# Kernel tuning notes

Hardware: AMD Instinct MI355X
Metric: run time of the kernel (lower is better)

## Reference

```python
import jax, jax.numpy as jnp
import numpy as np
from jax import lax

INPUT_SIZE = 16
RESERVOIR_SIZE = 1024
OUTPUT_SIZE = 16
SPECTRAL_RADIUS = 0.9
SPARSITY = 0.1
BATCH = 1024
SEQ_LEN = 4096


def setup_inputs() -> dict:
    key = jax.random.key(0)
    k_x, k_win, k_w, k_mask, k_wo, k_b = jax.random.split(key, 6)
    x = jax.random.normal(k_x, (BATCH, SEQ_LEN, INPUT_SIZE), dtype=jnp.float32)
    Win = jax.random.normal(k_win, (RESERVOIR_SIZE, INPUT_SIZE), dtype=jnp.float32)
    W = jax.random.normal(k_w, (RESERVOIR_SIZE, RESERVOIR_SIZE), dtype=jnp.float32)
    # spectral-radius rescaling (done once at init in the torch module)
    eig = np.linalg.eigvals(np.asarray(W))
    W = W * (SPECTRAL_RADIUS / np.max(np.abs(eig))).astype(np.float32)
    # sparsify with Bernoulli(sparsity) mask
    mask = (jax.random.uniform(k_mask, (RESERVOIR_SIZE, RESERVOIR_SIZE)) < SPARSITY).astype(jnp.float32)
    W = W * mask
    Wout_w = jax.random.normal(k_wo, (OUTPUT_SIZE, RESERVOIR_SIZE), dtype=jnp.float32) / np.sqrt(RESERVOIR_SIZE).astype(np.float32)
    Wout_b = jax.random.normal(k_b, (OUTPUT_SIZE,), dtype=jnp.float32) * 0.01
    return {"x": x, "Win": Win, "W": W, "Wout_w": Wout_w, "Wout_b": Wout_b}


def reference(x, Win, W, Wout_w, Wout_b):
    batch = x.shape[0]
    h0 = jnp.zeros((batch, W.shape[0]), dtype=x.dtype)

    def step(h, x_t):
        h = jnp.tanh(x_t @ Win.T + h @ W.T)
        return h, None

    # scan over time: x_time is [seq_len, batch, input_size]
    x_time = jnp.swapaxes(x, 0, 1)
    h_final, _ = lax.scan(step, h0, x_time)
    y = h_final @ Wout_w.T + Wout_b  # [batch, output_size]
    return y
```

## Files before the change

### kernel.cpp

```cpp
#include <hip/hip_runtime.h>

#define RS 1024
#define SL 4096
#define NB 1024
#define NI 16
#define RGRP 32
#define NGRP 32
#define WPG 8

typedef short s8v __attribute__((ext_vector_type(8)));
typedef float f16v __attribute__((ext_vector_type(16)));
typedef unsigned int u4v __attribute__((ext_vector_type(4)));

#define WAIT_VM(N) do { asm volatile("s_waitcnt vmcnt(" #N ")" ::: "memory"); \
                        __builtin_amdgcn_sched_barrier(0); } while (0)

static __device__ __forceinline__ unsigned short f2bf(float f) {
  unsigned u = __float_as_uint(f);
  u += 0x7fffu + ((u >> 16) & 1u);
  return (unsigned short)(u >> 16);
}
static __device__ __forceinline__ float bf2f(unsigned short b) {
  return __uint_as_float(((unsigned)b) << 16);
}
static __device__ __forceinline__ float fast_tanh(float a) {
  float e = __expf(2.0f * a);
  return 1.0f - 2.0f / (e + 1.0f);
}

static __device__ __forceinline__ u4v ld_llc_b128(const void* p) {
  u4v d;
  asm volatile("global_load_dwordx4 %0, %1, off sc0 sc1"
               : "=v"(d) : "v"(p) : "memory");
  return d;
}
static __device__ __forceinline__ void st_llc_b128(void* p, u4v d) {
  asm volatile("global_store_dwordx4 %0, %1, off sc0 sc1"
               : : "v"(p), "v"(d) : "memory");
}

__global__ __launch_bounds__(256) void prep_kernel(
    const float* __restrict__ W, unsigned short* __restrict__ wbf,
    uint4* __restrict__ hA4, int* __restrict__ flags) {
  int idx = blockIdx.x * 256 + threadIdx.x;
  if (idx < RS * RS) wbf[idx] = f2bf(W[idx]);
  if (idx < (NB * RS) / 8) hA4[idx] = make_uint4(0u, 0u, 0u, 0u);
  if (idx < NGRP * 64) flags[idx] = 0;
}

__global__ __launch_bounds__(256, 1) void esn_kernel(
    const float* __restrict__ x, const float* __restrict__ Win,
    const unsigned short* __restrict__ wbf,
    unsigned short* __restrict__ hA, unsigned short* __restrict__ hB,
    int* __restrict__ flags) {
  extern __shared__ char smem[];
  char* hsm = smem;
  char* ctile = smem + 65536;

  const int bid = blockIdx.x;
  const int g = bid & 31;
  const int j = bid >> 5;
  const int tid = threadIdx.x;
  const int w = tid >> 6;
  const int lane = tid & 63;
  const int l31 = lane & 31;
  const int hi = lane >> 5;

  const int n0 = j * 128 + w * 32;
  const int m0 = g * RGRP;

  s8v bw[64];
  {
    const unsigned short* wp = wbf + (size_t)(n0 + l31) * RS + hi * 8;
#pragma unroll
    for (int kk = 0; kk < 64; kk++) bw[kk] = *(const s8v*)(wp + kk * 16);
  }

  union U8 { s8v v; unsigned short u[8]; };
  U8 whi, wlo;
  {
    const float* p = Win + (n0 + l31) * NI + hi * 8;
#pragma unroll
    for (int i = 0; i < 8; i++) {
      float f = p[i];
      unsigned short h16 = f2bf(f);
      whi.u[i] = h16;
      wlo.u[i] = f2bf(f - bf2f(h16));
    }
  }

  int* flag = flags + g * 64;
  const float* xrow = x + (size_t)(m0 + l31) * SL * NI + hi * 8;
  const size_t stg_base = (((size_t)(tid >> 5) * NB) + m0 + (tid & 31)) << 4;
  const char* abase = hsm + hi * 512 + l31 * 16;
  char* wct = ctile + w * 2048;
  int dead = 0;

  for (int t = 0; t < SL; t++) {
    const char* hsrc = (const char*)((t & 1) ? hB : hA);
    char* hdst = (char*)((t & 1) ? hA : hB);

    float4 xa = *(const float4*)(xrow + (size_t)t * NI);
    float4 xb = *(const float4*)(xrow + (size_t)t * NI + 4);

    if (t > 0) {
      if (tid == 0 && !dead) {
        const int target = t * WPG;
        int spins = 0;
        while (__hip_atomic_load(flag, __ATOMIC_RELAXED, __HIP_MEMORY_SCOPE_AGENT) < target) {
          __builtin_amdgcn_s_sleep(8);
          if (++spins > (1 << 16)) { dead = 1; break; }
        }
      }
      __syncthreads();
    }

    {
      u4v stg[16];
#pragma unroll
      for (int q = 0; q < 16; q++)
        stg[q] = ld_llc_b128(hsrc + stg_base + (size_t)q * 131072);
      WAIT_VM(8);
#pragma unroll
      for (int q = 0; q < 8; q++)
        *(u4v*)(hsm + (tid << 4) + q * 4096) = stg[q];
      WAIT_VM(0);
#pragma unroll
      for (int q = 8; q < 16; q++)
        *(u4v*)(hsm + (tid << 4) + q * 4096) = stg[q];
    }

    U8 xhi, xlo;
    {
      float xf[8] = {xa.x, xa.y, xa.z, xa.w, xb.x, xb.y, xb.z, xb.w};
#pragma unroll
      for (int i = 0; i < 8; i++) {
        unsigned short h16 = f2bf(xf[i]);
        xhi.u[i] = h16;
        xlo.u[i] = f2bf(xf[i] - bf2f(h16));
      }
    }
    __syncthreads();

    f16v acc = {};
    acc = __builtin_amdgcn_mfma_f32_32x32x16_bf16(xhi.v, whi.v, acc, 0, 0, 0);
    acc = __builtin_amdgcn_mfma_f32_32x32x16_bf16(xlo.v, whi.v, acc, 0, 0, 0);
    acc = __builtin_amdgcn_mfma_f32_32x32x16_bf16(xhi.v, wlo.v, acc, 0, 0, 0);

#pragma unroll
    for (int kk = 0; kk < 64; kk++) {
      s8v a = *(const s8v*)(abase + kk * 1024);
      acc = __builtin_amdgcn_mfma_f32_32x32x16_bf16(a, bw[kk], acc, 0, 0, 0);
    }

#pragma unroll
    for (int r = 0; r < 16; r++) {
      const int row = (r & 3) + 8 * (r >> 2) + 4 * hi;
      *(unsigned short*)(wct + row * 64 + l31 * 2) = f2bf(fast_tanh(acc[r]));
    }
    asm volatile("s_waitcnt lgkmcnt(0)" ::: "memory");
    __builtin_amdgcn_sched_barrier(0);
    {
      const int row = lane >> 1, c = lane & 1;
      u4v v0 = *(const u4v*)(wct + row * 64 + c * 16);
      u4v v1 = *(const u4v*)(wct + row * 64 + c * 16 + 32);
      char* g0 = hdst + ((((size_t)(n0 >> 3) + c) * NB + m0 + row) << 4);
      char* g1 = hdst + ((((size_t)(n0 >> 3) + c + 2) * NB + m0 + row) << 4);
      st_llc_b128(g0, v0);
      st_llc_b128(g1, v1);
    }
    WAIT_VM(0);
    __syncthreads();
    if (tid == 0)
      __hip_atomic_fetch_add(flag, 1, __ATOMIC_RELAXED, __HIP_MEMORY_SCOPE_AGENT);
  }
}

__global__ __launch_bounds__(256) void yout_kernel(
    const unsigned short* __restrict__ h, const float* __restrict__ Wout,
    const float* __restrict__ bias, float* __restrict__ y) {
  const int tid = threadIdx.x;
  const int b = (blockIdx.x << 4) + (tid >> 4);
  const int o = tid & 15;
  const float* wr = Wout + (o << 10);
  float s = 0.0f;
  for (int k8 = 0; k8 < RS / 8; k8++) {
    const unsigned short* hc = h + (((size_t)k8 * NB + b) << 3);
#pragma unroll
    for (int i = 0; i < 8; i++) s += bf2f(hc[i]) * wr[k8 * 8 + i];
  }
  y[(b << 4) + o] = s + bias[o];
}

extern "C" void kernel_launch(void* const* d_in, const int* in_sizes, int n_in,
                              void* d_out, int out_size, void* d_ws, size_t ws_size,
                              hipStream_t stream) {
  const float* x = (const float*)d_in[0];
  const float* Win = (const float*)d_in[1];
  const float* W = (const float*)d_in[2];
  const float* Wout = (const float*)d_in[3];
  const float* bias = (const float*)d_in[4];
  float* y = (float*)d_out;

  char* ws = (char*)d_ws;
  unsigned short* hA = (unsigned short*)ws;
  unsigned short* hB = (unsigned short*)(ws + (1 << 21));
  unsigned short* wbf = (unsigned short*)(ws + (2 << 21));
  int* flags = (int*)(ws + 3 * (size_t)(1 << 21));

  (void)hipFuncSetAttribute((const void*)esn_kernel,
                            hipFuncAttributeMaxDynamicSharedMemorySize, 73728);

  prep_kernel<<<4096, 256, 0, stream>>>(W, wbf, (uint4*)hA, flags);
  esn_kernel<<<NGRP * WPG, 256, 73728, stream>>>(x, Win, wbf, hA, hB, flags);
  yout_kernel<<<64, 256, 0, stream>>>(hA, Wout, bias, y);
}
```

Baseline: 19.53 ms.

## Split K across waves and reduce partial sums through LDS instead of staging h

Each wave now loads only its quarter of the K dimension of h directly from global memory into registers, and computes partial products for all four 32-column output tiles. Partial accumulators are then exchanged through shared memory and summed by the owning wave. This removes the per-step copy of the full 32x1024 h tile into LDS and the repeated LDS reads of it. In exchange it adds an LDS reduction with extra stores and loads of floats, and it keeps four accumulators live, which raises register pressure.

```diff
diff --git a/kernel.cpp b/kernel.cpp
--- a/kernel.cpp
+++ b/kernel.cpp
@@ -54,7 +54,7 @@
     unsigned short* __restrict__ hA, unsigned short* __restrict__ hB,
     int* __restrict__ flags) {
   extern __shared__ char smem[];
-  char* hsm = smem;
+  char* psm = smem;
   char* ctile = smem + 65536;
 
   const int bid = blockIdx.x;
@@ -69,11 +69,14 @@
   const int n0 = j * 128 + w * 32;
   const int m0 = g * RGRP;
 
-  s8v bw[64];
-  {
-    const unsigned short* wp = wbf + (size_t)(n0 + l31) * RS + hi * 8;
-#pragma unroll
-    for (int kk = 0; kk < 64; kk++) bw[kk] = *(const s8v*)(wp + kk * 16);
+  s8v bw[4][16];
+#pragma unroll
+  for (int idx = 0; idx < 4; idx++) {
+    const int c = (w + idx) & 3;
+    const unsigned short* wp =
+        wbf + (size_t)(j * 128 + c * 32 + l31) * RS + w * 256 + hi * 8;
+#pragma unroll
+    for (int kk = 0; kk < 16; kk++) bw[idx][kk] = *(const s8v*)(wp + kk * 16);
   }
 
   union U8 { s8v v; unsigned short u[8]; };
@@ -91,8 +94,7 @@
 
   int* flag = flags + g * 64;
   const float* xrow = x + (size_t)(m0 + l31) * SL * NI + hi * 8;
-  const size_t stg_base = (((size_t)(tid >> 5) * NB) + m0 + (tid & 31)) << 4;
-  const char* abase = hsm + hi * 512 + l31 * 16;
+  const size_t ab_off = (((size_t)(32 * w + hi) * NB) + m0 + l31) << 4;
   char* wct = ctile + w * 2048;
   int dead = 0;
 
@@ -115,21 +117,6 @@
       __syncthreads();
     }
 
-    {
-      u4v stg[16];
-#pragma unroll
-      for (int q = 0; q < 16; q++)
-        stg[q] = ld_llc_b128(hsrc + stg_base + (size_t)q * 131072);
-      WAIT_VM(8);
-#pragma unroll
-      for (int q = 0; q < 8; q++)
-        *(u4v*)(hsm + (tid << 4) + q * 4096) = stg[q];
-      WAIT_VM(0);
-#pragma unroll
-      for (int q = 8; q < 16; q++)
-        *(u4v*)(hsm + (tid << 4) + q * 4096) = stg[q];
-    }
-
     U8 xhi, xlo;
     {
       float xf[8] = {xa.x, xa.y, xa.z, xa.w, xb.x, xb.y, xb.z, xb.w};
@@ -140,23 +127,61 @@
         xlo.u[i] = f2bf(xf[i] - bf2f(h16));
       }
     }
+    __builtin_amdgcn_sched_barrier(0);
+
+    u4v al[16];
+#pragma unroll
+    for (int kk = 0; kk < 16; kk++)
+      al[kk] = ld_llc_b128(hsrc + ab_off + (size_t)kk * (2 * NB * 16));
+
+    f16v acc[4];
+    {
+      f16v z = {};
+      z = __builtin_amdgcn_mfma_f32_32x32x16_bf16(xhi.v, whi.v, z, 0, 0, 0);
+      z = __builtin_amdgcn_mfma_f32_32x32x16_bf16(xlo.v, whi.v, z, 0, 0, 0);
+      acc[0] = __builtin_amdgcn_mfma_f32_32x32x16_bf16(xhi.v, wlo.v, z, 0, 0, 0);
+      f16v zz = {};
+      acc[1] = zz; acc[2] = zz; acc[3] = zz;
+    }
+
+#define KBLK(K0)                                                            \
+    _Pragma("unroll")                                                       \
+    for (int kk = K0; kk < K0 + 4; kk++) {                                  \
+      union AU { u4v u; s8v s; } au; au.u = al[kk];                         \
+      _Pragma("unroll")                                                     \
+      for (int idx = 0; idx < 4; idx++)                                     \
+        acc[idx] = __builtin_amdgcn_mfma_f32_32x32x16_bf16(au.s, bw[idx][kk], acc[idx], 0, 0, 0); \
+    }
+    WAIT_VM(12); KBLK(0)
+    WAIT_VM(8);  KBLK(4)
+    WAIT_VM(4);  KBLK(8)
+    WAIT_VM(0);  KBLK(12)
+#undef KBLK
+
+#pragma unroll
+    for (int idx = 1; idx < 4; idx++) {
+      const int c = (w + idx) & 3;
+      char* slot = psm + (((c << 2) | w) << 12) + (size_t)l31 * 4;
+#pragma unroll
+      for (int r = 0; r < 16; r++)
+        *(float*)(slot + (hi * 16 + r) * 128) = acc[idx][r];
+    }
     __syncthreads();
 
-    f16v acc = {};
-    acc = __builtin_amdgcn_mfma_f32_32x32x16_bf16(xhi.v, whi.v, acc, 0, 0, 0);
-    acc = __builtin_amdgcn_mfma_f32_32x32x16_bf16(xlo.v, whi.v, acc, 0, 0, 0);
-    acc = __builtin_amdgcn_mfma_f32_32x32x16_bf16(xhi.v, wlo.v, acc, 0, 0, 0);
-
-#pragma unroll
-    for (int kk = 0; kk < 64; kk++) {
-      s8v a = *(const s8v*)(abase + kk * 1024);
-      acc = __builtin_amdgcn_mfma_f32_32x32x16_bf16(a, bw[kk], acc, 0, 0, 0);
+    f16v own = acc[0];
+#pragma unroll
+    for (int idx = 1; idx < 4; idx++) {
+      const int wp = (w + idx) & 3;
+      const char* slot = psm + (((w << 2) | wp) << 12) + (size_t)l31 * 4;
+#pragma unroll
+      for (int r = 0; r < 16; r++)
+        own[r] += *(const float*)(slot + (hi * 16 + r) * 128);
     }
 
 #pragma unroll
     for (int r = 0; r < 16; r++) {
       const int row = (r & 3) + 8 * (r >> 2) + 4 * hi;
-      *(unsigned short*)(wct + row * 64 + l31 * 2) = f2bf(fast_tanh(acc[r]));
+      *(unsigned short*)(wct + row * 64 + l31 * 2) = f2bf(fast_tanh(own[r]));
     }
     asm volatile("s_waitcnt lgkmcnt(0)" ::: "memory");
     __builtin_amdgcn_sched_barrier(0);
```

Result: faster. 17.76 ms (-9.1%).

## Restructure ESN recurrence into two interleaved batch halves with split-K partial reduction

Applied to the files above, without the earlier changes.

Cuts the grid from 256 to 128 blocks. Each block now handles two 32-row batch tiles, one from each half of the batch, and alternates between them so the epilogue and global stores of one tile overlap the MFMA stream of the other. Each wave now takes a K-quarter for all four column chunks and loads h fragments straight from global into registers instead of staging them through LDS. Partial sums are reduced through LDS. Per-tile counters and centralized atomic increments are replaced by per-block flag stores polled on only the two producer blocks each wave needs, which adds LDS reduction traffic and more complex synchronization.

```diff
diff --git a/kernel.cpp b/kernel.cpp
--- a/kernel.cpp
+++ b/kernel.cpp
@@ -4,16 +4,15 @@
 #define SL 4096
 #define NB 1024
 #define NI 16
-#define RGRP 32
-#define NGRP 32
+#define NGP 16
 #define WPG 8
 
 typedef short s8v __attribute__((ext_vector_type(8)));
 typedef float f16v __attribute__((ext_vector_type(16)));
 typedef unsigned int u4v __attribute__((ext_vector_type(4)));
 
-#define WAIT_VM(N) do { asm volatile("s_waitcnt vmcnt(" #N ")" ::: "memory"); \
-                        __builtin_amdgcn_sched_barrier(0); } while (0)
+#define WAIT_VM0 do { asm volatile("s_waitcnt vmcnt(0)" ::: "memory"); \
+                      __builtin_amdgcn_sched_barrier(0); } while (0)
 
 static __device__ __forceinline__ unsigned short f2bf(float f) {
   unsigned u = __float_as_uint(f);
@@ -37,6 +36,16 @@
 static __device__ __forceinline__ void st_llc_b128(void* p, u4v d) {
   asm volatile("global_store_dwordx4 %0, %1, off sc0 sc1"
                : : "v"(p), "v"(d) : "memory");
+}
+static __device__ __forceinline__ void st_llc_b32(void* p, int d) {
+  asm volatile("global_store_dword %0, %1, off sc0 sc1"
+               : : "v"(p), "v"(d) : "memory");
+}
+static __device__ __forceinline__ int ld_llc_b32(const void* p) {
+  int d;
+  asm volatile("global_load_dword %0, %1, off sc0 sc1\n\ts_waitcnt vmcnt(0)"
+               : "=v"(d) : "v"(p) : "memory");
+  return d;
 }
 
 __global__ __launch_bounds__(256) void prep_kernel(
@@ -45,21 +54,21 @@
   int idx = blockIdx.x * 256 + threadIdx.x;
   if (idx < RS * RS) wbf[idx] = f2bf(W[idx]);
   if (idx < (NB * RS) / 8) hA4[idx] = make_uint4(0u, 0u, 0u, 0u);
-  if (idx < NGRP * 64) flags[idx] = 0;
+  if (idx < 4096) flags[idx] = 0;
 }
 
 __global__ __launch_bounds__(256, 1) void esn_kernel(
     const float* __restrict__ x, const float* __restrict__ Win,
     const unsigned short* __restrict__ wbf,
-    unsigned short* __restrict__ hA, unsigned short* __restrict__ hB,
+    unsigned short* __restrict__ h0, unsigned short* __restrict__ h1,
     int* __restrict__ flags) {
   extern __shared__ char smem[];
-  char* hsm = smem;
+  char* psm = smem;
   char* ctile = smem + 65536;
 
   const int bid = blockIdx.x;
-  const int g = bid & 31;
-  const int j = bid >> 5;
+  const int p = bid & 15;
+  const int j = bid >> 4;
   const int tid = threadIdx.x;
   const int w = tid >> 6;
   const int lane = tid & 63;
@@ -67,113 +76,184 @@
   const int hi = lane >> 5;
 
   const int n0 = j * 128 + w * 32;
-  const int m0 = g * RGRP;
-
-  s8v bw[64];
-  {
-    const unsigned short* wp = wbf + (size_t)(n0 + l31) * RS + hi * 8;
-#pragma unroll
-    for (int kk = 0; kk < 64; kk++) bw[kk] = *(const s8v*)(wp + kk * 16);
+  const int m0A = p * 32;
+  const int m0B = m0A + 512;
+
+  s8v bw[4][16];
+#pragma unroll
+  for (int idx = 0; idx < 4; idx++) {
+    const int c = (w + idx) & 3;
+    const unsigned short* wp =
+        wbf + (size_t)(j * 128 + c * 32 + l31) * RS + w * 256 + hi * 8;
+#pragma unroll
+    for (int kk = 0; kk < 16; kk++) bw[idx][kk] = *(const s8v*)(wp + kk * 16);
   }
 
   union U8 { s8v v; unsigned short u[8]; };
   U8 whi, wlo;
   {
-    const float* p = Win + (n0 + l31) * NI + hi * 8;
+    const float* q = Win + (n0 + l31) * NI + hi * 8;
 #pragma unroll
     for (int i = 0; i < 8; i++) {
-      float f = p[i];
+      float f = q[i];
       unsigned short h16 = f2bf(f);
       whi.u[i] = h16;
       wlo.u[i] = f2bf(f - bf2f(h16));
     }
   }
 
-  int* flag = flags + g * 64;
-  const float* xrow = x + (size_t)(m0 + l31) * SL * NI + hi * 8;
-  const size_t stg_base = (((size_t)(tid >> 5) * NB) + m0 + (tid & 31)) << 4;
-  const char* abase = hsm + hi * 512 + l31 * 16;
+  int* flagsA = flags;
+  int* flagsB = flags + 2048;
+  int* myfA = flagsA + ((p * WPG + j) << 4);
+  int* myfB = flagsB + ((p * WPG + j) << 4);
+  const int* pfA0 = flagsA + ((p * WPG + 2 * w) << 4);
+  const int* pfA1 = flagsA + ((p * WPG + 2 * w + 1) << 4);
+  const int* pfB0 = flagsB + ((p * WPG + 2 * w) << 4);
+  const int* pfB1 = flagsB + ((p * WPG + 2 * w + 1) << 4);
+
+  const float* xrowA = x + (size_t)(m0A + l31) * SL * NI + hi * 8;
+  const float* xrowB = x + (size_t)(m0B + l31) * SL * NI + hi * 8;
+  const size_t abA = (((size_t)(32 * w + hi) * NB) + m0A + l31) << 4;
+  const size_t abB = abA + ((size_t)512 << 4);
   char* wct = ctile + w * 2048;
   int dead = 0;
 
-  for (int t = 0; t < SL; t++) {
-    const char* hsrc = (const char*)((t & 1) ? hB : hA);
-    char* hdst = (char*)((t & 1) ? hA : hB);
-
-    float4 xa = *(const float4*)(xrow + (size_t)t * NI);
-    float4 xb = *(const float4*)(xrow + (size_t)t * NI + 4);
-
-    if (t > 0) {
-      if (tid == 0 && !dead) {
-        const int target = t * WPG;
-        int spins = 0;
-        while (__hip_atomic_load(flag, __ATOMIC_RELAXED, __HIP_MEMORY_SCOPE_AGENT) < target) {
-          __builtin_amdgcn_s_sleep(8);
-          if (++spins > (1 << 16)) { dead = 1; break; }
-        }
-      }
-      __syncthreads();
+#define POLL(F0, F1, TGT)                                                   \
+  if (lane == 0 && !dead) {                                                 \
+    int spins = 0;                                                          \
+    while (ld_llc_b32(F0) < (TGT) || ld_llc_b32(F1) < (TGT)) {              \
+      __builtin_amdgcn_s_sleep(2);                                          \
+      if (++spins > (1 << 14)) { dead = 1; break; }                         \
+    }                                                                       \
+  }
+
+#define ISSUE_AL(AL, SRC, AB)                                               \
+  _Pragma("unroll")                                                         \
+  for (int kk = 0; kk < 16; kk++)                                           \
+    AL[kk] = ld_llc_b128((SRC) + (AB) + (size_t)kk * (2 * NB * 16));
+
+#define XFRAG(XA0, XA1, XH, XL)                                             \
+  {                                                                         \
+    float xf[8] = {XA0.x, XA0.y, XA0.z, XA0.w, XA1.x, XA1.y, XA1.z, XA1.w}; \
+    _Pragma("unroll")                                                       \
+    for (int i = 0; i < 8; i++) {                                           \
+      unsigned short h16 = f2bf(xf[i]);                                     \
+      XH.u[i] = h16;                                                        \
+      XL.u[i] = f2bf(xf[i] - bf2f(h16));                                    \
+    }                                                                       \
+  }
+
+#define MFMA_STREAM(AL, XH, XL, ACC)                                        \
+  {                                                                         \
+    f16v z = {};                                                            \
+    z = __builtin_amdgcn_mfma_f32_32x32x16_bf16(XH.v, whi.v, z, 0, 0, 0);   \
+    z = __builtin_amdgcn_mfma_f32_32x32x16_bf16(XL.v, whi.v, z, 0, 0, 0);   \
+    ACC[0] = __builtin_amdgcn_mfma_f32_32x32x16_bf16(XH.v, wlo.v, z, 0, 0, 0); \
+    f16v zz = {};                                                           \
+    ACC[1] = zz; ACC[2] = zz; ACC[3] = zz;                                  \
+  }                                                                         \
+  _Pragma("unroll")                                                         \
+  for (int kk = 0; kk < 16; kk++) {                                         \
+    union AU { u4v u; s8v s; } au; au.u = AL[kk];                           \
+    _Pragma("unroll")                                                       \
+    for (int idx = 0; idx < 4; idx++)                                       \
+      ACC[idx] = __builtin_amdgcn_mfma_f32_32x32x16_bf16(au.s, bw[idx][kk], ACC[idx], 0, 0, 0); \
+  }
+
+#define PARTIAL_WRITE(ACC)                                                  \
+  _Pragma("unroll")                                                         \
+  for (int idx = 1; idx < 4; idx++) {                                       \
+    const int c = (w + idx) & 3;                                            \
+    char* slot = psm + (((c << 2) | w) << 12) + (size_t)l31 * 4;            \
+    _Pragma("unroll")                                                       \
+    for (int r = 0; r < 16; r++)                                            \
+      *(float*)(slot + (hi * 16 + r) * 128) = ACC[idx][r];                  \
+  }
+
+#define REDUCE_EPI(ACC, M0, HD)                                             \
+  {                                                                         \
+    f16v own = ACC[0];                                                      \
+    _Pragma("unroll")                                                       \
+    for (int idx = 1; idx < 4; idx++) {                                     \
+      const int wp2 = (w + idx) & 3;                                        \
+      const char* slot = psm + (((w << 2) | wp2) << 12) + (size_t)l31 * 4;  \
+      _Pragma("unroll")                                                     \
+      for (int r = 0; r < 16; r++)                                          \
+        own[r] += *(const float*)(slot + (hi * 16 + r) * 128);              \
+    }                                                                       \
+    _Pragma("unroll")                                                       \
+    for (int r = 0; r < 16; r++) {                                          \
+      const int row = (r & 3) + 8 * (r >> 2) + 4 * hi;                      \
+      *(unsigned short*)(wct + row * 64 + l31 * 2) = f2bf(fast_tanh(own[r])); \
+    }                                                                       \
+    asm volatile("s_waitcnt lgkmcnt(0)" ::: "memory");                      \
+    __builtin_amdgcn_sched_barrier(0);                                      \
+    const int row = lane >> 1, c = lane & 1;                                \
+    u4v v0 = *(const u4v*)(wct + row * 64 + c * 16);                        \
+    u4v v1 = *(const u4v*)(wct + row * 64 + c * 16 + 32);                   \
+    char* g0 = (HD) + ((((size_t)(n0 >> 3) + c) * NB + (M0) + row) << 4);   \
+    char* g1 = (HD) + ((((size_t)(n0 >> 3) + c + 2) * NB + (M0) + row) << 4); \
+    st_llc_b128(g0, v0);                                                    \
+    st_llc_b128(g1, v1);                                                    \
+  }
+
+  u4v alA[16], alB[16];
+  float4 xa0, xa1, xb0, xb1;
+  ISSUE_AL(alB, (const char*)h0, abB)
+  ISSUE_AL(alA, (const char*)h0, abA)
+  xa0 = *(const float4*)(xrowA);
+  xa1 = *(const float4*)(xrowA + 4);
+  xb0 = *(const float4*)(xrowB);
+  xb1 = *(const float4*)(xrowB + 4);
+
+  for (int it = 0; it < SL; it++) {
+    const char* hsrc = (const char*)((it & 1) ? h1 : h0);
+    char* hdst = (char*)((it & 1) ? h0 : h1);
+    (void)hsrc;
+
+    WAIT_VM0;
+    U8 xh, xl;
+    XFRAG(xa0, xa1, xh, xl)
+    f16v acc[4];
+    MFMA_STREAM(alA, xh, xl, acc)
+
+    PARTIAL_WRITE(acc)
+    __syncthreads();
+    REDUCE_EPI(acc, m0A, hdst)
+
+    XFRAG(xb0, xb1, xh, xl)
+    MFMA_STREAM(alB, xh, xl, acc)
+    __syncthreads();
+
+    PARTIAL_WRITE(acc)
+    WAIT_VM0;
+    __syncthreads();
+    if (tid == 0) st_llc_b32(myfA, it + 1);
+    REDUCE_EPI(acc, m0B, hdst)
+
+    POLL(pfA0, pfA1, it + 1)
+
+    WAIT_VM0;
+    __syncthreads();
+    if (tid == 0) st_llc_b32(myfB, it + 1);
+
+    POLL(pfB0, pfB1, it + 1)
+    ISSUE_AL(alB, hdst, abB)
+    ISSUE_AL(alA, hdst, abA)
+    {
+      const size_t xo = (size_t)((it + 1 < SL) ? it + 1 : 0) * NI;
+      xa0 = *(const float4*)(xrowA + xo);
+      xa1 = *(const float4*)(xrowA + xo + 4);
+      xb0 = *(const float4*)(xrowB + xo);
+      xb1 = *(const float4*)(xrowB + xo + 4);
     }
-
-    {
-      u4v stg[16];
-#pragma unroll
-      for (int q = 0; q < 16; q++)
-        stg[q] = ld_llc_b128(hsrc + stg_base + (size_t)q * 131072);
-      WAIT_VM(8);
-#pragma unroll
-      for (int q = 0; q < 8; q++)
-        *(u4v*)(hsm + (tid << 4) + q * 4096) = stg[q];
-      WAIT_VM(0);
-#pragma unroll
-      for (int q = 8; q < 16; q++)
-        *(u4v*)(hsm + (tid << 4) + q * 4096) = stg[q];
-    }
-
-    U8 xhi, xlo;
-    {
-      float xf[8] = {xa.x, xa.y, xa.z, xa.w, xb.x, xb.y, xb.z, xb.w};
-#pragma unroll
-      for (int i = 0; i < 8; i++) {
-        unsigned short h16 = f2bf(xf[i]);
-        xhi.u[i] = h16;
-        xlo.u[i] = f2bf(xf[i] - bf2f(h16));
-      }
-    }
-    __syncthreads();
-
-    f16v acc = {};
-    acc = __builtin_amdgcn_mfma_f32_32x32x16_bf16(xhi.v, whi.v, acc, 0, 0, 0);
-    acc = __builtin_amdgcn_mfma_f32_32x32x16_bf16(xlo.v, whi.v, acc, 0, 0, 0);
-    acc = __builtin_amdgcn_mfma_f32_32x32x16_bf16(xhi.v, wlo.v, acc, 0, 0, 0);
-
-#pragma unroll
-    for (int kk = 0; kk < 64; kk++) {
-      s8v a = *(const s8v*)(abase + kk * 1024);
-      acc = __builtin_amdgcn_mfma_f32_32x32x16_bf16(a, bw[kk], acc, 0, 0, 0);
-    }
-
-#pragma unroll
-    for (int r = 0; r < 16; r++) {
-      const int row = (r & 3) + 8 * (r >> 2) + 4 * hi;
-      *(unsigned short*)(wct + row * 64 + l31 * 2) = f2bf(fast_tanh(acc[r]));
-    }
-    asm volatile("s_waitcnt lgkmcnt(0)" ::: "memory");
-    __builtin_amdgcn_sched_barrier(0);
-    {
-      const int row = lane >> 1, c = lane & 1;
-      u4v v0 = *(const u4v*)(wct + row * 64 + c * 16);
-      u4v v1 = *(const u4v*)(wct + row * 64 + c * 16 + 32);
-      char* g0 = hdst + ((((size_t)(n0 >> 3) + c) * NB + m0 + row) << 4);
-      char* g1 = hdst + ((((size_t)(n0 >> 3) + c + 2) * NB + m0 + row) << 4);
-      st_llc_b128(g0, v0);
-      st_llc_b128(g1, v1);
-    }
-    WAIT_VM(0);
-    __syncthreads();
-    if (tid == 0)
-      __hip_atomic_fetch_add(flag, 1, __ATOMIC_RELAXED, __HIP_MEMORY_SCOPE_AGENT);
-  }
+  }
+#undef POLL
+#undef ISSUE_AL
+#undef XFRAG
+#undef MFMA_STREAM
+#undef PARTIAL_WRITE
+#undef REDUCE_EPI
 }
 
 __global__ __launch_bounds__(256) void yout_kernel(
@@ -203,15 +283,15 @@
   float* y = (float*)d_out;
 
   char* ws = (char*)d_ws;
-  unsigned short* hA = (unsigned short*)ws;
-  unsigned short* hB = (unsigned short*)(ws + (1 << 21));
+  unsigned short* h0 = (unsigned short*)ws;
+  unsigned short* h1 = (unsigned short*)(ws + (1 << 21));
   unsigned short* wbf = (unsigned short*)(ws + (2 << 21));
   int* flags = (int*)(ws + 3 * (size_t)(1 << 21));
 
   (void)hipFuncSetAttribute((const void*)esn_kernel,
                             hipFuncAttributeMaxDynamicSharedMemorySize, 73728);
 
-  prep_kernel<<<4096, 256, 0, stream>>>(W, wbf, (uint4*)hA, flags);
-  esn_kernel<<<NGRP * WPG, 256, 73728, stream>>>(x, Win, wbf, hA, hB, flags);
-  yout_kernel<<<64, 256, 0, stream>>>(hA, Wout, bias, y);
-}
+  prep_kernel<<<4096, 256, 0, stream>>>(W, wbf, (uint4*)h0, flags);
+  esn_kernel<<<NGP * WPG, 256, 73728, stream>>>(x, Win, wbf, h0, h1, flags);
+  yout_kernel<<<64, 256, 0, stream>>>(h0, Wout, bias, y);
+}
```

Measured after the change: 55.89 ms. 2.86x slower.

## Split-K recurrence with two interleaved batch halves and per-wave flag polling

Applied to the files above, without the earlier changes.

Restructures the persistent ESN kernel so each block owns 64 output columns for 16 partitions, with waves splitting the K dimension and reducing partials through LDS. The batch is split into two halves processed alternately, so the global-memory load of one half's state overlaps the compute and sync of the other. Hidden-state fragments are loaded directly from global memory into registers, skipping the LDS staging step. The single atomic counter per group is replaced by per-wave flag words polled with vector loads. This aims to hide the step-to-step sync latency, at the cost of the LDS reduction and a more complex flag protocol.

```diff
diff --git a/kernel.cpp b/kernel.cpp
--- a/kernel.cpp
+++ b/kernel.cpp
@@ -4,9 +4,6 @@
 #define SL 4096
 #define NB 1024
 #define NI 16
-#define RGRP 32
-#define NGRP 32
-#define WPG 8
 
 typedef short s8v __attribute__((ext_vector_type(8)));
 typedef float f16v __attribute__((ext_vector_type(16)));
@@ -34,146 +31,241 @@
                : "=v"(d) : "v"(p) : "memory");
   return d;
 }
+static __device__ __forceinline__ u4v ld_llc_b128_sync(const void* p) {
+  u4v d;
+  asm volatile("global_load_dwordx4 %0, %1, off sc0 sc1\n\ts_waitcnt vmcnt(0)"
+               : "=v"(d) : "v"(p) : "memory");
+  return d;
+}
 static __device__ __forceinline__ void st_llc_b128(void* p, u4v d) {
   asm volatile("global_store_dwordx4 %0, %1, off sc0 sc1"
                : : "v"(p), "v"(d) : "memory");
 }
+static __device__ __forceinline__ void st_llc_b32(void* p, int d) {
+  asm volatile("global_store_dword %0, %1, off sc0 sc1"
+               : : "v"(p), "v"(d) : "memory");
+}
+static __device__ __forceinline__ int min16v(u4v a, u4v b, u4v c, u4v d) {
+  int m = min(min(min((int)a.x, (int)a.y), min((int)a.z, (int)a.w)),
+              min(min((int)b.x, (int)b.y), min((int)b.z, (int)b.w)));
+  int n = min(min(min((int)c.x, (int)c.y), min((int)c.z, (int)c.w)),
+              min(min((int)d.x, (int)d.y), min((int)d.z, (int)d.w)));
+  return min(m, n);
+}
+static __device__ __forceinline__ void poll_issue(const void* p, u4v& a, u4v& b,
+                                                  u4v& c, u4v& d) {
+  asm volatile("global_load_dwordx4 %0, %4, off sc0 sc1\n\t"
+               "global_load_dwordx4 %1, %4, off offset:16 sc0 sc1\n\t"
+               "global_load_dwordx4 %2, %4, off offset:32 sc0 sc1\n\t"
+               "global_load_dwordx4 %3, %4, off offset:48 sc0 sc1"
+               : "=v"(a), "=v"(b), "=v"(c), "=v"(d) : "v"(p) : "memory");
+}
+static __device__ __forceinline__ int min16_block(const void* p) {
+  u4v a, b, c, d;
+  asm volatile("global_load_dwordx4 %0, %4, off sc0 sc1\n\t"
+               "global_load_dwordx4 %1, %4, off offset:16 sc0 sc1\n\t"
+               "global_load_dwordx4 %2, %4, off offset:32 sc0 sc1\n\t"
+               "global_load_dwordx4 %3, %4, off offset:48 sc0 sc1\n\t"
+               "s_waitcnt vmcnt(0)"
+               : "=v"(a), "=v"(b), "=v"(c), "=v"(d) : "v"(p) : "memory");
+  return min16v(a, b, c, d);
+}
 
 __global__ __launch_bounds__(256) void prep_kernel(
     const float* __restrict__ W, unsigned short* __restrict__ wbf,
-    uint4* __restrict__ hA4, int* __restrict__ flags) {
+    char* __restrict__ h0, int* __restrict__ flags) {
   int idx = blockIdx.x * 256 + threadIdx.x;
   if (idx < RS * RS) wbf[idx] = f2bf(W[idx]);
-  if (idx < (NB * RS) / 8) hA4[idx] = make_uint4(0u, 0u, 0u, 0u);
-  if (idx < NGRP * 64) flags[idx] = 0;
+  if (idx < (NB * RS) / 8) {
+    u4v z = {0u, 0u, 0u, 0u};
+    st_llc_b128(h0 + (size_t)idx * 16, z);
+  }
+  if (idx < 2048) st_llc_b32(flags + idx, 0);
 }
 
 __global__ __launch_bounds__(256, 1) void esn_kernel(
     const float* __restrict__ x, const float* __restrict__ Win,
     const unsigned short* __restrict__ wbf,
-    unsigned short* __restrict__ hA, unsigned short* __restrict__ hB,
+    unsigned short* __restrict__ h0, unsigned short* __restrict__ h1,
     int* __restrict__ flags) {
   extern __shared__ char smem[];
-  char* hsm = smem;
+  char* slA = smem;
+  char* slB = smem + 32768;
   char* ctile = smem + 65536;
 
   const int bid = blockIdx.x;
-  const int g = bid & 31;
-  const int j = bid >> 5;
+  const int p = bid & 15;
+  const int j = bid >> 4;
   const int tid = threadIdx.x;
   const int w = tid >> 6;
   const int lane = tid & 63;
   const int l31 = lane & 31;
   const int hi = lane >> 5;
-
-  const int n0 = j * 128 + w * 32;
-  const int m0 = g * RGRP;
-
-  s8v bw[64];
-  {
-    const unsigned short* wp = wbf + (size_t)(n0 + l31) * RS + hi * 8;
-#pragma unroll
-    for (int kk = 0; kk < 64; kk++) bw[kk] = *(const s8v*)(wp + kk * 16);
+  const int tw = w & 1;
+  const int rq = w >> 1;
+  const int colbase = j * 64;
+  const int n0t = colbase + tw * 32;
+
+  s8v bw[2][16];
+#pragma unroll
+  for (int c = 0; c < 2; c++) {
+    const unsigned short* wp =
+        wbf + (size_t)(colbase + c * 32 + l31) * RS + w * 256 + hi * 8;
+#pragma unroll
+    for (int kk = 0; kk < 16; kk++) bw[c][kk] = *(const s8v*)(wp + kk * 16);
   }
 
   union U8 { s8v v; unsigned short u[8]; };
   U8 whi, wlo;
   {
-    const float* p = Win + (n0 + l31) * NI + hi * 8;
+    const float* q = Win + (n0t + l31) * NI + hi * 8;
 #pragma unroll
     for (int i = 0; i < 8; i++) {
-      float f = p[i];
+      float f = q[i];
       unsigned short h16 = f2bf(f);
       whi.u[i] = h16;
       wlo.u[i] = f2bf(f - bf2f(h16));
     }
   }
 
-  int* flag = flags + g * 64;
-  const float* xrow = x + (size_t)(m0 + l31) * SL * NI + hi * 8;
-  const size_t stg_base = (((size_t)(tid >> 5) * NB) + m0 + (tid & 31)) << 4;
-  const char* abase = hsm + hi * 512 + l31 * 16;
-  char* wct = ctile + w * 2048;
-  int dead = 0;
+  int* flA = flags + p * 64;
+  int* flB = flags + 1024 + p * 64;
+  int* myfA = flA + j * 4 + w;
+  int* myfB = flB + j * 4 + w;
+  const int* plA = flA + 16 * w;
+  const int* plB = flB + 16 * w;
+
+  const float* xrA = x + (size_t)(p * 32 + l31) * SL * NI + hi * 8;
+  const float* xrB = xrA + (size_t)512 * SL * NI;
+  const size_t abA = (((size_t)(32 * w + hi) * NB) + p * 32 + l31) << 4;
+  const size_t abB = abA + ((size_t)512 << 4);
+  const int c8l = lane >> 4, rloc = lane & 15;
+  const size_t stA =
+      ((((size_t)(j * 8 + tw * 4 + c8l)) * NB) + p * 32 + rq * 16 + rloc) << 4;
+  const size_t stB = stA + ((size_t)512 << 4);
+  char* wct = ctile + w * 1024;
+  int dead = 0, spins = 0;
+
+#define KBLK4(K0)                                                              \
+  _Pragma("unroll") for (int kk = K0; kk < K0 + 4; kk++) {                     \
+    union AU { u4v u; s8v s; } au; au.u = al[kk];                              \
+    acc0 = __builtin_amdgcn_mfma_f32_32x32x16_bf16(au.s, bw[0][kk], acc0, 0, 0, 0); \
+    acc1 = __builtin_amdgcn_mfma_f32_32x32x16_bf16(au.s, bw[1][kk], acc1, 0, 0, 0); \
+  }
+#define PROJ(X0, X1)                                                           \
+  {                                                                            \
+    U8 xh, xl;                                                                 \
+    float xf[8] = {X0.x, X0.y, X0.z, X0.w, X1.x, X1.y, X1.z, X1.w};            \
+    _Pragma("unroll") for (int i = 0; i < 8; i++) {                            \
+      unsigned short h16 = f2bf(xf[i]);                                        \
+      xh.u[i] = h16; xl.u[i] = f2bf(xf[i] - bf2f(h16));                        \
+    }                                                                          \
+    f16v z = {};                                                               \
+    z = __builtin_amdgcn_mfma_f32_32x32x16_bf16(xh.v, whi.v, z, 0, 0, 0);      \
+    z = __builtin_amdgcn_mfma_f32_32x32x16_bf16(xl.v, whi.v, z, 0, 0, 0);      \
+    proj = __builtin_amdgcn_mfma_f32_32x32x16_bf16(xh.v, wlo.v, z, 0, 0, 0);   \
+  }
+#define PARTIALS(SLOT)                                                         \
+  _Pragma("unroll") for (int r = 0; r < 16; r++)                               \
+    *(float*)((SLOT) + (w << 12) + l31 * 4 + (hi * 16 + r) * 128) = acc0[r];   \
+  _Pragma("unroll") for (int r = 0; r < 16; r++)                               \
+    *(float*)((SLOT) + ((4 + w) << 12) + l31 * 4 + (hi * 16 + r) * 128) = acc1[r];
+#define REDUCE(SLOT)                                                           \
+  _Pragma("unroll") for (int rr = 0; rr < 8; rr++) {                           \
+    float s = 0.f;                                                             \
+    _Pragma("unroll") for (int pr = 0; pr < 4; pr++)                           \
+      s += *(const float*)((SLOT) + ((tw * 4 + pr) << 12) + l31 * 4 +          \
+                           (hi * 16 + rq * 8 + rr) * 128);                     \
+    own[rr] = s;                                                               \
+  }
+#define EPILOGUE(STOFF, DST)                                                   \
+  {                                                                            \
+    if (rq == 0) { _Pragma("unroll") for (int rr = 0; rr < 8; rr++) own[rr] += proj[rr]; } \
+    else { _Pragma("unroll") for (int rr = 0; rr < 8; rr++) own[rr] += proj[8 + rr]; } \
+    _Pragma("unroll") for (int rr = 0; rr < 8; rr++) {                         \
+      const int rl = (rr & 3) + 8 * (rr >> 2) + 4 * hi;                        \
+      *(unsigned short*)(wct + rl * 64 + l31 * 2) = f2bf(fast_tanh(own[rr]));  \
+    }                                                                          \
+    asm volatile("s_waitcnt lgkmcnt(0)" ::: "memory");                         \
+    __builtin_amdgcn_sched_barrier(0);                                         \
+    u4v v = *(const u4v*)(wct + rloc * 64 + c8l * 16);                         \
+    st_llc_b128((DST) + (STOFF), v);                                           \
+  }
+#define POLLCHK(PL, TGT)                                                       \
+  if (!dead) {                                                                 \
+    int m = min16v(q0, q1, q2, q3);                                            \
+    while (m < (TGT)) {                                                        \
+      __builtin_amdgcn_s_sleep(2);                                             \
+      if (++spins > (1 << 14)) { dead = 1; break; }                            \
+      m = min16_block(PL);                                                     \
+    }                                                                          \
+  }
+
+  u4v al[16];
+#pragma unroll
+  for (int kk = 0; kk < 16; kk++)
+    al[kk] = ld_llc_b128((const char*)h0 + abA + (size_t)kk * (2 * NB * 16));
+  float4 xa0 = *(const float4*)xrA, xa1 = *(const float4*)(xrA + 4);
+  float4 xb0 = *(const float4*)xrB, xb1 = *(const float4*)(xrB + 4);
+  if (lane == 0) st_llc_b32(myfB, 0);
 
   for (int t = 0; t < SL; t++) {
-    const char* hsrc = (const char*)((t & 1) ? hB : hA);
-    char* hdst = (char*)((t & 1) ? hA : hB);
-
-    float4 xa = *(const float4*)(xrow + (size_t)t * NI);
-    float4 xb = *(const float4*)(xrow + (size_t)t * NI + 4);
-
-    if (t > 0) {
-      if (tid == 0 && !dead) {
-        const int target = t * WPG;
-        int spins = 0;
-        while (__hip_atomic_load(flag, __ATOMIC_RELAXED, __HIP_MEMORY_SCOPE_AGENT) < target) {
-          __builtin_amdgcn_s_sleep(8);
-          if (++spins > (1 << 16)) { dead = 1; break; }
-        }
-      }
-      __syncthreads();
+    const char* src = (const char*)((t & 1) ? h1 : h0);
+    char* dst = (char*)((t & 1) ? h0 : h1);
+
+    f16v acc0 = {}, acc1 = {};
+    WAIT_VM(17); KBLK4(0)
+    WAIT_VM(13); KBLK4(4)
+    WAIT_VM(9);  KBLK4(8)
+    WAIT_VM(5);  KBLK4(12)
+    WAIT_VM(1);
+    f16v proj;
+    PROJ(xa0, xa1)
+    PARTIALS(slA)
+    __syncthreads();
+    u4v q0, q1, q2, q3;
+    poll_issue(plB, q0, q1, q2, q3);
+    float own[8];
+    REDUCE(slA)
+    WAIT_VM(0);
+    POLLCHK(plB, t)
+    EPILOGUE(stA, dst)
+#pragma unroll
+    for (int kk = 0; kk < 16; kk++)
+      al[kk] = ld_llc_b128(src + abB + (size_t)kk * (2 * NB * 16));
+    WAIT_VM(16);
+    if (lane == 0) st_llc_b32(myfA, t + 1);
+
+    acc0 = {}; acc1 = {};
+    WAIT_VM(13); KBLK4(0)
+    WAIT_VM(9);  KBLK4(4)
+    WAIT_VM(5);  KBLK4(8)
+    WAIT_VM(1);  KBLK4(12)
+    PROJ(xb0, xb1)
+    PARTIALS(slB)
+    __syncthreads();
+    poll_issue(plA, q0, q1, q2, q3);
+    REDUCE(slB)
+    WAIT_VM(0);
+    POLLCHK(plA, t + 1)
+    EPILOGUE(stB, dst)
+#pragma unroll
+    for (int kk = 0; kk < 16; kk++)
+      al[kk] = ld_llc_b128((const char*)dst + abA + (size_t)kk * (2 * NB * 16));
+    {
+      const size_t xo = (size_t)((t + 1 < SL) ? t + 1 : 0) * NI;
+      xa0 = *(const float4*)(xrA + xo); xa1 = *(const float4*)(xrA + xo + 4);
+      xb0 = *(const float4*)(xrB + xo); xb1 = *(const float4*)(xrB + xo + 4);
     }
-
-    {
-      u4v stg[16];
-#pragma unroll
-      for (int q = 0; q < 16; q++)
-        stg[q] = ld_llc_b128(hsrc + stg_base + (size_t)q * 131072);
-      WAIT_VM(8);
-#pragma unroll
-      for (int q = 0; q < 8; q++)
-        *(u4v*)(hsm + (tid << 4) + q * 4096) = stg[q];
-      WAIT_VM(0);
-#pragma unroll
-      for (int q = 8; q < 16; q++)
-        *(u4v*)(hsm + (tid << 4) + q * 4096) = stg[q];
-    }
-
-    U8 xhi, xlo;
-    {
-      float xf[8] = {xa.x, xa.y, xa.z, xa.w, xb.x, xb.y, xb.z, xb.w};
-#pragma unroll
-      for (int i = 0; i < 8; i++) {
-        unsigned short h16 = f2bf(xf[i]);
-        xhi.u[i] = h16;
-        xlo.u[i] = f2bf(xf[i] - bf2f(h16));
-      }
-    }
-    __syncthreads();
-
-    f16v acc = {};
-    acc = __builtin_amdgcn_mfma_f32_32x32x16_bf16(xhi.v, whi.v, acc, 0, 0, 0);
-    acc = __builtin_amdgcn_mfma_f32_32x32x16_bf16(xlo.v, whi.v, acc, 0, 0, 0);
-    acc = __builtin_amdgcn_mfma_f32_32x32x16_bf16(xhi.v, wlo.v, acc, 0, 0, 0);
-
-#pragma unroll
-    for (int kk = 0; kk < 64; kk++) {
-      s8v a = *(const s8v*)(abase + kk * 1024);
-      acc = __builtin_amdgcn_mfma_f32_32x32x16_bf16(a, bw[kk], acc, 0, 0, 0);
-    }
-
-#pragma unroll
-    for (int r = 0; r < 16; r++) {
-      const int row = (r & 3) + 8 * (r >> 2) + 4 * hi;
-      *(unsigned short*)(wct + row * 64 + l31 * 2) = f2bf(fast_tanh(acc[r]));
-    }
-    asm volatile("s_waitcnt lgkmcnt(0)" ::: "memory");
-    __builtin_amdgcn_sched_barrier(0);
-    {
-      const int row = lane >> 1, c = lane & 1;
-      u4v v0 = *(const u4v*)(wct + row * 64 + c * 16);
-      u4v v1 = *(const u4v*)(wct + row * 64 + c * 16 + 32);
-      char* g0 = hdst + ((((size_t)(n0 >> 3) + c) * NB + m0 + row) << 4);
-      char* g1 = hdst + ((((size_t)(n0 >> 3) + c + 2) * NB + m0 + row) << 4);
-      st_llc_b128(g0, v0);
-      st_llc_b128(g1, v1);
-    }
-    WAIT_VM(0);
-    __syncthreads();
-    if (tid == 0)
-      __hip_atomic_fetch_add(flag, 1, __ATOMIC_RELAXED, __HIP_MEMORY_SCOPE_AGENT);
-  }
+    WAIT_VM(20);
+    if (lane == 0) st_llc_b32(myfB, t + 1);
+  }
+#undef KBLK4
+#undef PROJ
+#undef PARTIALS
+#undef REDUCE
+#undef EPILOGUE
+#undef POLLCHK
 }
 
 __global__ __launch_bounds__(256) void yout_kernel(
@@ -185,9 +277,10 @@
   const float* wr = Wout + (o << 10);
   float s = 0.0f;
   for (int k8 = 0; k8 < RS / 8; k8++) {
-    const unsigned short* hc = h + (((size_t)k8 * NB + b) << 3);
-#pragma unroll
-    for (int i = 0; i < 8; i++) s += bf2f(hc[i]) * wr[k8 * 8 + i];
+    union { u4v u; unsigned short us[8]; } uu;
+    uu.u = ld_llc_b128_sync((const char*)h + (((size_t)k8 * NB + b) << 4));
+#pragma unroll
+    for (int i = 0; i < 8; i++) s += bf2f(uu.us[i]) * wr[k8 * 8 + i];
   }
   y[(b << 4) + o] = s + bias[o];
 }
@@ -203,15 +296,15 @@
   float* y = (float*)d_out;
 
   char* ws = (char*)d_ws;
-  unsigned short* hA = (unsigned short*)ws;
-  unsigned short* hB = (unsigned short*)(ws + (1 << 21));
+  unsigned short* h0 = (unsigned short*)ws;
+  unsigned short* h1 = (unsigned short*)(ws + (1 << 21));
   unsigned short* wbf = (unsigned short*)(ws + (2 << 21));
   int* flags = (int*)(ws + 3 * (size_t)(1 << 21));
 
   (void)hipFuncSetAttribute((const void*)esn_kernel,
-                            hipFuncAttributeMaxDynamicSharedMemorySize, 73728);
-
-  prep_kernel<<<4096, 256, 0, stream>>>(W, wbf, (uint4*)hA, flags);
-  esn_kernel<<<NGRP * WPG, 256, 73728, stream>>>(x, Win, wbf, hA, hB, flags);
-  yout_kernel<<<64, 256, 0, stream>>>(hA, Wout, bias, y);
-}
+                            hipFuncAttributeMaxDynamicSharedMemorySize, 69632);
+
+  prep_kernel<<<4096, 256, 0, stream>>>(W, wbf, (char*)h0, flags);
+  esn_kernel<<<256, 256, 69632, stream>>>(x, Win, wbf, h0, h1, flags);
+  yout_kernel<<<64, 256, 0, stream>>>(h0, Wout, bias, y);
+}
```

After: 19.56 ms. No clear change (+0.2%).
